# Kernel tuning notes

Measured on AMD Instinct MI355X. Metric: run time of the kernel, lower is better.

Reference implementation:

```python
import jax, jax.numpy as jnp
import numpy as np
import math

NUM_HEADS = 16
ROPE_BASE = 10000.0
SLIDING_WINDOW = 512  # note: original triu-then-tril composition makes the mask empty (no-op)


def _rope_cos_sin(seq_len, head_dim, dtype):
    inv_freq = 1.0 / (ROPE_BASE ** (jnp.arange(0, head_dim, 2, dtype=jnp.float32) / head_dim))
    t = jnp.arange(seq_len, dtype=jnp.float32)
    freqs = t[:, None] * inv_freq[None, :]          # [S, D/2]
    emb = jnp.concatenate([freqs, freqs], axis=-1)  # [S, D]
    # reshape to broadcast over [B, S, H, D]
    return jnp.cos(emb)[None, :, None, :].astype(dtype), jnp.sin(emb)[None, :, None, :].astype(dtype)


def _rotate_half(x):
    x1, x2 = jnp.split(x, 2, axis=-1)
    return jnp.concatenate([-x2, x1], axis=-1)


def setup_inputs() -> dict:
    key = jax.random.key(0)
    ks = jax.random.split(key, 9)
    B, S, E = 2, 2048, 2048
    sc = 1.0 / math.sqrt(E)
    return {
        "hidden_states": jax.random.normal(ks[0], (B, S, E), dtype=jnp.float32),
        "Wq": jax.random.normal(ks[1], (E, E), dtype=jnp.float32) * sc,
        "bq": jax.random.normal(ks[2], (E,), dtype=jnp.float32) * 0.01,
        "Wk": jax.random.normal(ks[3], (E, E), dtype=jnp.float32) * sc,
        "bk": jax.random.normal(ks[4], (E,), dtype=jnp.float32) * 0.01,
        "Wv": jax.random.normal(ks[5], (E, E), dtype=jnp.float32) * sc,
        "bv": jax.random.normal(ks[6], (E,), dtype=jnp.float32) * 0.01,
        "Wo": jax.random.normal(ks[7], (E, E), dtype=jnp.float32) * sc,
        "bo": jax.random.normal(ks[8], (E,), dtype=jnp.float32) * 0.01,
    }


def reference(hidden_states, Wq, bq, Wk, bk, Wv, bv, Wo, bo):
    B, S, E = hidden_states.shape
    H = NUM_HEADS
    D = E // H
    q = (hidden_states @ Wq.T + bq).reshape(B, S, H, D)
    k = (hidden_states @ Wk.T + bk).reshape(B, S, H, D)
    v = (hidden_states @ Wv.T + bv).reshape(B, S, H, D)

    cos, sin = _rope_cos_sin(S, D, q.dtype)
    q = q * cos + _rotate_half(q) * sin
    k = k * cos + _rotate_half(k) * sin

    scale = 1.0 / math.sqrt(D)
    scores = jnp.einsum("bqhd,bkhd->bhqk", q, k) * scale  # [B,H,S,S]
    # Faithful to source: triu(ones, +w) followed by tril(..., -w) is empty -> mask is a no-op.
    attn = jax.nn.softmax(scores, axis=-1)
    out = jnp.einsum("bhqk,bkhd->bqhd", attn, v).reshape(B, S, E)
    return out @ Wo.T + bo
```

## Files before the change

### kernel.cpp

```cpp
#include <hip/hip_runtime.h>
#include <hip/hip_bf16.h>

#define B_ 2
#define S_ 2048
#define E_ 2048
#define H_ 16
#define D_ 128
#define M_ (B_*S_)
#define NQKV_ (3*E_)

typedef __attribute__((ext_vector_type(8))) short bf16x8;
typedef __attribute__((ext_vector_type(4))) float f32x4;
typedef __attribute__((ext_vector_type(4))) unsigned short u16x4;
typedef __attribute__((ext_vector_type(2))) unsigned u32x2;

__device__ __forceinline__ unsigned short f2bf(float f) {
  union { float f; unsigned u; } v; v.f = f;
  unsigned r = v.u + 0x7fffu + ((v.u >> 16) & 1u);
  return (unsigned short)(r >> 16);
}
__device__ __forceinline__ float bf2f(unsigned short h) {
  union { unsigned u; float f; } v; v.u = ((unsigned)h) << 16;
  return v.f;
}

__device__ __forceinline__ void gload_lds16(const void* g, void* l) {
  __builtin_amdgcn_global_load_lds(
      (const __attribute__((address_space(1))) unsigned*)g,
      (__attribute__((address_space(3))) unsigned*)l, 16, 0, 0);
}

__global__ __launch_bounds__(256) void prep_kernel(
    const float* __restrict__ hs,
    const float* __restrict__ Wq, const float* __restrict__ Wk, const float* __restrict__ Wv,
    const float* __restrict__ Wo,
    const float* __restrict__ bq, const float* __restrict__ bk, const float* __restrict__ bv,
    unsigned short* __restrict__ hsb, unsigned short* __restrict__ Wqkv,
    unsigned short* __restrict__ Wob, float* __restrict__ biasqkv,
    float* __restrict__ cosT, float* __restrict__ sinT)
{
  const int seg = blockIdx.y;
  const int t0 = blockIdx.x * 256 + threadIdx.x;
  const int stride = gridDim.x * 256;
  if (seg == 0) {
    const int n = (M_*E_)/4;
    for (int i = t0; i < n; i += stride) {
      f32x4 v = ((const f32x4*)hs)[i];
      u16x4 o; o[0]=f2bf(v[0]); o[1]=f2bf(v[1]); o[2]=f2bf(v[2]); o[3]=f2bf(v[3]);
      ((u16x4*)hsb)[i] = o;
    }
  } else if (seg == 1) {
    const int n = (3*E_*E_)/4;
    for (int i = t0; i < n; i += stride) {
      int e4 = i << 2;
      int r = e4 >> 11;
      int k = e4 & 2047;
      const float* src = (r < E_) ? (Wq + ((size_t)r << 11) + k)
                       : (r < 2*E_) ? (Wk + ((size_t)(r - E_) << 11) + k)
                       : (Wv + ((size_t)(r - 2*E_) << 11) + k);
      f32x4 v = *(const f32x4*)src;
      u16x4 o; o[0]=f2bf(v[0]); o[1]=f2bf(v[1]); o[2]=f2bf(v[2]); o[3]=f2bf(v[3]);
      ((u16x4*)Wqkv)[i] = o;
    }
  } else if (seg == 2) {
    const int n = (E_*E_)/4;
    for (int i = t0; i < n; i += stride) {
      f32x4 v = ((const f32x4*)Wo)[i];
      u16x4 o; o[0]=f2bf(v[0]); o[1]=f2bf(v[1]); o[2]=f2bf(v[2]); o[3]=f2bf(v[3]);
      ((u16x4*)Wob)[i] = o;
    }
  } else if (seg == 3) {
    for (int i = t0; i < NQKV_; i += stride)
      biasqkv[i] = (i < E_) ? bq[i] : (i < 2*E_) ? bk[i - E_] : bv[i - 2*E_];
  } else {
    for (int i = t0; i < S_*64; i += stride) {
      int j = i & 63, s = i >> 6;
      float inv = exp2f(-(float)j * (13.287712379549449f / 64.0f));
      float ang = (float)s * inv;
      cosT[i] = cosf(ang);
      sinT[i] = sinf(ang);
    }
  }
}

#define STAGE8(basePtr, BUF, AB, KS, KT) do { \
    unsigned short* dst_ = lds + (BUF)*32768 + (AB)*16384 + (KS)*8192; \
    const unsigned short* src_ = (basePtr) + (KT)*64 + (KS)*32; \
    _Pragma("unroll") \
    for (int j_ = 0; j_ < 2; ++j_) { \
      int cc_ = (j_ << 9) + tid; \
      int row_ = cc_ >> 2, c2_ = cc_ & 3; \
      int sc_ = c2_ ^ ((row_ >> 1) & 3); \
      gload_lds16(src_ + (size_t)row_*K + sc_*8, (char*)dst_ + cc_*16); \
    } } while(0)

#define LOADA8(DST, MH, KS, BUF) do { \
    const unsigned short* Ab_ = lds + (BUF)*32768 + (KS)*8192; \
    _Pragma("unroll") \
    for (int j_ = 0; j_ < 4; ++j_) { \
      int row_ = wr*128 + ((MH)*4 + j_)*16 + l15; \
      DST[j_] = *(const bf16x8*)(Ab_ + row_*32 + ((l4 ^ ((row_>>1)&3)) << 3)); \
    } } while(0)

#define LOADB8(DST, KS, BUF) do { \
    const unsigned short* Bb_ = lds + (BUF)*32768 + 16384 + (KS)*8192; \
    _Pragma("unroll") \
    for (int j_ = 0; j_ < 4; ++j_) { \
      int row_ = wc*64 + j_*16 + l15; \
      DST[j_] = *(const bf16x8*)(Bb_ + row_*32 + ((l4 ^ ((row_>>1)&3)) << 3)); \
    } } while(0)

#define PRIO_MFMA(MH, AF, BF) do { \
    __builtin_amdgcn_s_setprio(1); \
    _Pragma("unroll") \
    for (int mm_ = 0; mm_ < 4; ++mm_) \
      _Pragma("unroll") \
      for (int nn_ = 0; nn_ < 4; ++nn_) \
        acc[(MH)*4+mm_][nn_] = __builtin_amdgcn_mfma_f32_16x16x32_bf16(AF[mm_], BF[nn_], acc[(MH)*4+mm_][nn_], 0,0,0); \
    __builtin_amdgcn_s_setprio(0); \
  } while(0)

#define BARPIN do { \
    __builtin_amdgcn_sched_barrier(0); \
    __builtin_amdgcn_s_barrier(); \
    __builtin_amdgcn_sched_barrier(0); \
  } while(0)

__global__ __launch_bounds__(512, 2) void gemm8(
    const unsigned short* __restrict__ A,
    const unsigned short* __restrict__ Bm,
    const float* __restrict__ bias,
    unsigned short* __restrict__ Cv,
    int M, int N, int K)
{
  __shared__ __align__(16) unsigned short lds[65536];
  const int tid = threadIdx.x;
  const int lane = tid & 63;
  const int w = tid >> 6;
  const int wr = w >> 2, wc = w & 3;
  const int l15 = lane & 15, l4 = lane >> 4;

  const int ntile = N >> 8;
  int wg = blockIdx.x;
  const int cpx = gridDim.x >> 3;
  wg = (wg & 7) * cpx + (wg >> 3);
  const int tm = wg / ntile, tn = wg % ntile;

  const unsigned short* Abase = A + ((size_t)tm*256)*K;
  const unsigned short* Bbase = Bm + ((size_t)tn*256)*K;

  f32x4 acc[8][4] = {};
  bf16x8 afA[4], afB[4], bfA[4], bfB[4];

  const int NITER = K >> 7;

  STAGE8(Bbase, 0, 1, 0, 0); STAGE8(Abase, 0, 0, 0, 0);
  STAGE8(Bbase, 0, 1, 1, 0); STAGE8(Abase, 0, 0, 1, 0);
  STAGE8(Bbase, 1, 1, 0, 1); STAGE8(Abase, 1, 0, 0, 1);
  STAGE8(Bbase, 1, 1, 1, 1);
  __builtin_amdgcn_sched_barrier(0);
  asm volatile("s_waitcnt vmcnt(6)" ::: "memory");
  __builtin_amdgcn_s_barrier();
  __builtin_amdgcn_sched_barrier(0);

  for (int i = 0; i < NITER; ++i) {
    const int t1k = 2*i + 1, t2k = 2*i + 2, t3k = 2*i + 3;
    const bool nl = (i < NITER - 1);
    STAGE8(Abase, 1, 0, 1, t1k);
    LOADA8(afA, 0, 0, 0); LOADB8(bfA, 0, 0);
    LOADA8(afB, 1, 0, 0);
    PRIO_MFMA(0, afA, bfA);
    BARPIN;
    if (nl) STAGE8(Bbase, 0, 1, 0, t2k);
    LOADA8(afA, 0, 1, 0); LOADB8(bfB, 1, 0);
    PRIO_MFMA(1, afB, bfA);
    BARPIN;
    if (nl) STAGE8(Abase, 0, 0, 0, t2k);
    LOADA8(afB, 1, 1, 0);
    PRIO_MFMA(0, afA, bfB);
    BARPIN;
    if (nl) STAGE8(Bbase, 0, 1, 1, t2k);
    PRIO_MFMA(1, afB, bfB);
    __builtin_amdgcn_sched_barrier(0);
    if (nl) asm volatile("s_waitcnt vmcnt(6)" ::: "memory");
    else    asm volatile("s_waitcnt vmcnt(0)" ::: "memory");
    __builtin_amdgcn_s_barrier();
    __builtin_amdgcn_sched_barrier(0);
    if (nl) STAGE8(Abase, 0, 0, 1, t2k);
    LOADA8(afA, 0, 0, 1); LOADB8(bfA, 0, 1);
    LOADA8(afB, 1, 0, 1);
    PRIO_MFMA(0, afA, bfA);
    BARPIN;
    if (nl) STAGE8(Bbase, 1, 1, 0, t3k);
    LOADA8(afA, 0, 1, 1); LOADB8(bfB, 1, 1);
    PRIO_MFMA(1, afB, bfA);
    BARPIN;
    if (nl) STAGE8(Abase, 1, 0, 0, t3k);
    LOADA8(afB, 1, 1, 1);
    PRIO_MFMA(0, afA, bfB);
    BARPIN;
    if (nl) STAGE8(Bbase, 1, 1, 1, t3k);
    PRIO_MFMA(1, afB, bfB);
    __builtin_amdgcn_sched_barrier(0);
    if (nl) asm volatile("s_waitcnt vmcnt(6)" ::: "memory");
    else    asm volatile("s_waitcnt vmcnt(0)" ::: "memory");
    __builtin_amdgcn_s_barrier();
    __builtin_amdgcn_sched_barrier(0);
  }

  #pragma unroll
  for (int mt = 0; mt < 8; ++mt) {
    #pragma unroll
    for (int nt = 0; nt < 4; ++nt) {
      int colg = tn*256 + wc*64 + nt*16 + l15;
      float bvv = bias[colg];
      #pragma unroll
      for (int r = 0; r < 4; ++r) {
        int rowg = tm*256 + wr*128 + mt*16 + l4*4 + r;
        Cv[(size_t)rowg*N + colg] = f2bf(acc[mt][nt][r] + bvv);
      }
    }
  }
}

template<int OUT_F32>
__global__ __launch_bounds__(256) void gemm_bt(
    const unsigned short* __restrict__ A,
    const unsigned short* __restrict__ Bm,
    const float* __restrict__ bias,
    void* __restrict__ Cv,
    int M, int N, int K)
{
  __shared__ unsigned short lA[128*64];
  __shared__ unsigned short lB[128*64];
  const int tid = threadIdx.x;
  const int lane = tid & 63;
  const int w = tid >> 6;
  const int wr = w >> 1, wc = w & 1;
  const int ntile = N >> 7;
  const int tm = blockIdx.x / ntile, tn = blockIdx.x % ntile;
  const int l15 = lane & 15, l4 = lane >> 4;

  f32x4 acc[4][4] = {};

  for (int kt = 0; kt < K; kt += 64) {
    #pragma unroll
    for (int i = 0; i < 4; ++i) {
      int cc = i*256 + tid;
      int row = cc >> 3, col = cc & 7;
      int scol = col ^ (row & 7);
      gload_lds16(A + (size_t)(tm*128 + row)*K + kt + scol*8, (char*)lA + cc*16);
    }
    #pragma unroll
    for (int i = 0; i < 4; ++i) {
      int cc = i*256 + tid;
      int row = cc >> 3, col = cc & 7;
      int scol = col ^ (row & 7);
      gload_lds16(Bm + (size_t)(tn*128 + row)*K + kt + scol*8, (char*)lB + cc*16);
    }
    asm volatile("s_waitcnt vmcnt(0)" ::: "memory");
    __syncthreads();

    #pragma unroll
    for (int ks = 0; ks < 2; ++ks) {
      bf16x8 af[4], bfr[4];
      #pragma unroll
      for (int mt = 0; mt < 4; ++mt) {
        int row = wr*64 + mt*16 + l15;
        int ch = (ks*4 + l4) ^ (row & 7);
        af[mt] = *(const bf16x8*)(lA + row*64 + ch*8);
      }
      #pragma unroll
      for (int nt = 0; nt < 4; ++nt) {
        int row = wc*64 + nt*16 + l15;
        int ch = (ks*4 + l4) ^ (row & 7);
        bfr[nt] = *(const bf16x8*)(lB + row*64 + ch*8);
      }
      #pragma unroll
      for (int mt = 0; mt < 4; ++mt)
        #pragma unroll
        for (int nt = 0; nt < 4; ++nt)
          acc[mt][nt] = __builtin_amdgcn_mfma_f32_16x16x32_bf16(af[mt], bfr[nt], acc[mt][nt], 0, 0, 0);
    }
    __syncthreads();
  }

  #pragma unroll
  for (int mt = 0; mt < 4; ++mt) {
    #pragma unroll
    for (int nt = 0; nt < 4; ++nt) {
      int colg = tn*128 + wc*64 + nt*16 + l15;
      float bvv = bias[colg];
      #pragma unroll
      for (int r = 0; r < 4; ++r) {
        int rowg = tm*128 + wr*64 + mt*16 + l4*4 + r;
        float v = acc[mt][nt][r] + bvv;
        if (OUT_F32) ((float*)Cv)[(size_t)rowg*N + colg] = v;
        else ((unsigned short*)Cv)[(size_t)rowg*N + colg] = f2bf(v);
      }
    }
  }
}

__global__ __launch_bounds__(256) void rope_kernel(
    unsigned short* __restrict__ qkv, const float* __restrict__ cosT, const float* __restrict__ sinT)
{
  int t = blockIdx.x*256 + threadIdx.x;
  int i  = t & 63;
  int h  = (t >> 6) & 15;
  int m  = t >> 10;
  int s  = m & (S_-1);
  float c = cosT[s*64 + i], sn = sinT[s*64 + i];
  const float scale = 0.08838834764831845f * 1.4426950408889634f;
  size_t base = (size_t)m*NQKV_ + h*128;
  float q1 = bf2f(qkv[base+i]), q2 = bf2f(qkv[base+64+i]);
  qkv[base+i]    = f2bf((q1*c - q2*sn)*scale);
  qkv[base+64+i] = f2bf((q2*c + q1*sn)*scale);
  size_t kb = base + E_;
  float k1 = bf2f(qkv[kb+i]), k2 = bf2f(qkv[kb+64+i]);
  qkv[kb+i]    = f2bf(k1*c - k2*sn);
  qkv[kb+64+i] = f2bf(k2*c + k1*sn);
}

__global__ __launch_bounds__(256) void transv_kernel(
    const unsigned short* __restrict__ qkv, unsigned short* __restrict__ Vt)
{
  __shared__ unsigned short t[32][33];
  int bid = blockIdx.x;
  int st = bid & 63;
  int dt = (bid >> 6) & 3;
  int bh = bid >> 8;
  int b = bh >> 4, h = bh & 15;
  int tx = threadIdx.x & 31, ty = threadIdx.x >> 5;
  #pragma unroll
  for (int j = 0; j < 4; ++j) {
    int r = ty + j*8;
    t[r][tx] = qkv[(size_t)(b*S_ + st*32 + r)*NQKV_ + 2*E_ + h*128 + dt*32 + tx];
  }
  __syncthreads();
  #pragma unroll
  for (int j = 0; j < 4; ++j) {
    int r = ty + j*8;
    Vt[((size_t)bh*D_ + dt*32 + r)*S_ + st*32 + tx] = t[tx][r];
  }
}

__global__ __launch_bounds__(256, 4) void attn_kernel(
    const unsigned short* __restrict__ qkv, const unsigned short* __restrict__ Vt,
    unsigned short* __restrict__ Ao)
{
  __shared__ unsigned short lK[64*128];
  __shared__ unsigned short lV[128*64];
  __shared__ __align__(16) unsigned short lP[4*16*64];
  const int bid = blockIdx.x;
  const int qt = bid & 31;
  const int bh = bid >> 5;
  const int b = bh >> 4, h = bh & 15;
  const int tid = threadIdx.x, lane = tid & 63, w = tid >> 6;
  const int l15 = lane & 15, l4 = lane >> 4;

  const int qrow = qt*64 + w*16 + l15;
  const unsigned short* qp = qkv + (size_t)(b*S_ + qrow)*NQKV_ + h*128 + l4*8;
  bf16x8 qf[4];
  #pragma unroll
  for (int f = 0; f < 4; ++f) qf[f] = *(const bf16x8*)(qp + f*32);

  f32x4 O[8];
  #pragma unroll
  for (int i = 0; i < 8; ++i) O[i] = (f32x4){0.f,0.f,0.f,0.f};
  float m = -1e30f, lsum = 0.f;

  unsigned short* myP = lP + w*(16*64);
  const int ksw = (l15 & 7) << 3;
  const size_t kbase = (size_t)b*S_*NQKV_ + E_ + (size_t)h*128;
  const size_t vbase = (size_t)bh*D_*S_;

  for (int kt = 0; kt < S_; kt += 64) {
    #pragma unroll
    for (int i = 0; i < 4; ++i) {
      int cc = i*256 + tid;
      int row = cc >> 4, col = cc & 15;
      int scol = col ^ (row & 7);
      gload_lds16(qkv + kbase + (size_t)(kt + row)*NQKV_ + scol*8, (char*)lK + cc*16);
    }
    #pragma unroll
    for (int i = 0; i < 4; ++i) {
      int cc = i*256 + tid;
      int row = cc >> 3, col = cc & 7;
      int scol = col ^ ((row & 7) ^ ((row >> 3) & 7));
      gload_lds16(Vt + vbase + (size_t)row*S_ + kt + scol*8, (char*)lV + cc*16);
    }
    asm volatile("s_waitcnt vmcnt(0)" ::: "memory");
    __syncthreads();

    f32x4 sfr[4];
    #pragma unroll
    for (int nf = 0; nf < 4; ++nf) {
      f32x4 s = (f32x4){0.f,0.f,0.f,0.f};
      #pragma unroll
      for (int ks = 0; ks < 4; ++ks) {
        int row = nf*16 + l15;
        int ch = (ks*4 + l4) ^ (row & 7);
        bf16x8 kf = *(const bf16x8*)(lK + row*128 + ch*8);
        s = __builtin_amdgcn_mfma_f32_16x16x32_bf16(kf, qf[ks], s, 0, 0, 0);
      }
      sfr[nf] = s;
    }

    float vmax = -1e30f;
    #pragma unroll
    for (int nf = 0; nf < 4; ++nf)
      #pragma unroll
      for (int r = 0; r < 4; ++r) vmax = fmaxf(vmax, sfr[nf][r]);
    vmax = fmaxf(vmax, __shfl_xor(vmax, 16, 64));
    vmax = fmaxf(vmax, __shfl_xor(vmax, 32, 64));

    if (__any(vmax > m + 8.0f)) {
      float mn = fmaxf(m, vmax);
      float al = __builtin_amdgcn_exp2f(m - mn);
      m = mn;
      lsum *= al;
      #pragma unroll
      for (int r = 0; r < 4; ++r) {
        float ar = __shfl(al, (lane & 48) + l4*4 + r, 64);
        #pragma unroll
        for (int df = 0; df < 8; ++df) O[df][r] *= ar;
      }
    }

    float ps = 0.f;
    #pragma unroll
    for (int nf = 0; nf < 4; ++nf) {
      #pragma unroll
      for (int r = 0; r < 4; ++r) {
        float p = __builtin_amdgcn_exp2f(sfr[nf][r] - m);
        sfr[nf][r] = p;
        ps += p;
      }
    }
    ps += __shfl_xor(ps, 16, 64);
    ps += __shfl_xor(ps, 32, 64);
    lsum += ps;

    #pragma unroll
    for (int nf = 0; nf < 4; ++nf) {
      unsigned lo = (unsigned)f2bf(sfr[nf][0]) | ((unsigned)f2bf(sfr[nf][1]) << 16);
      unsigned hi = (unsigned)f2bf(sfr[nf][2]) | ((unsigned)f2bf(sfr[nf][3]) << 16);
      int k0 = (nf*16 + l4*4) ^ ksw;
      u32x2 val; val[0] = lo; val[1] = hi;
      *(u32x2*)(myP + l15*64 + k0) = val;
    }
    asm volatile("s_waitcnt lgkmcnt(0)" ::: "memory");

    #pragma unroll
    for (int ks2 = 0; ks2 < 2; ++ks2) {
      int kk = (ks2*32 + l4*8) ^ ksw;
      bf16x8 pf = *(const bf16x8*)(myP + l15*64 + kk);
      #pragma unroll
      for (int df = 0; df < 8; ++df) {
        int row = df*16 + l15;
        int ch = (ks2*4 + l4) ^ ((row & 7) ^ ((row >> 3) & 7));
        bf16x8 vf = *(const bf16x8*)(lV + row*64 + ch*8);
        O[df] = __builtin_amdgcn_mfma_f32_16x16x32_bf16(pf, vf, O[df], 0, 0, 0);
      }
    }
    __syncthreads();
  }

  float linv = 1.0f / lsum;
  float inv[4];
  #pragma unroll
  for (int r = 0; r < 4; ++r) inv[r] = __shfl(linv, (lane & 48) + l4*4 + r, 64);
  #pragma unroll
  for (int df = 0; df < 8; ++df) {
    int colg = h*128 + df*16 + l15;
    #pragma unroll
    for (int r = 0; r < 4; ++r) {
      int rowg = qt*64 + w*16 + l4*4 + r;
      Ao[(size_t)(b*S_ + rowg)*E_ + colg] = f2bf(O[df][r] * inv[r]);
    }
  }
}

extern "C" void kernel_launch(void* const* d_in, const int* in_sizes, int n_in,
                              void* d_out, int out_size, void* d_ws, size_t ws_size,
                              hipStream_t stream) {
  const float* hs = (const float*)d_in[0];
  const float* Wq = (const float*)d_in[1];
  const float* bq = (const float*)d_in[2];
  const float* Wk = (const float*)d_in[3];
  const float* bk = (const float*)d_in[4];
  const float* Wv = (const float*)d_in[5];
  const float* bv = (const float*)d_in[6];
  const float* Wo = (const float*)d_in[7];
  const float* bo = (const float*)d_in[8];
  float* out = (float*)d_out;

  char* p = (char*)d_ws;
  auto alloc = [&](size_t bytes) { char* r = p; p += (bytes + 255) & ~(size_t)255; return r; };
  unsigned short* hsb  = (unsigned short*)alloc((size_t)M_*E_*2);
  unsigned short* Wqkv = (unsigned short*)alloc((size_t)NQKV_*E_*2);
  unsigned short* Wob  = (unsigned short*)alloc((size_t)E_*E_*2);
  unsigned short* qkv  = (unsigned short*)alloc((size_t)M_*NQKV_*2);
  unsigned short* Vt   = (unsigned short*)alloc((size_t)B_*H_*D_*S_*2);
  unsigned short* Ao   = (unsigned short*)alloc((size_t)M_*E_*2);
  float* biasqkv = (float*)alloc((size_t)NQKV_*4);
  float* cosT = (float*)alloc((size_t)S_*64*4);
  float* sinT = (float*)alloc((size_t)S_*64*4);

  prep_kernel<<<dim3(2048, 5), 256, 0, stream>>>(hs, Wq, Wk, Wv, Wo, bq, bk, bv,
      hsb, Wqkv, Wob, biasqkv, cosT, sinT);
  gemm8<<<dim3((M_/256)*(NQKV_/256)), 512, 0, stream>>>(hsb, Wqkv, biasqkv, qkv, M_, NQKV_, E_);
  rope_kernel<<<dim3((M_*H_*64)/256), 256, 0, stream>>>(qkv, cosT, sinT);
  transv_kernel<<<dim3(B_*H_*(D_/32)*(S_/32)), 256, 0, stream>>>(qkv, Vt);
  attn_kernel<<<dim3(B_*H_*(S_/64)), 256, 0, stream>>>(qkv, Vt, Ao);
  gemm_bt<1><<<dim3((M_/128)*(E_/128)), 256, 0, stream>>>(Ao, Wob, bo, out, M_, E_, E_);
}
```

Before: 318.1 us.

## Double attention query tile per block to reuse K/V LDS tiles

Each wave now processes two 16-row query groups instead of one, so a block covers 128 query rows and every K/V tile loaded into LDS feeds twice the MFMA work. This halves the global-to-LDS traffic per query row and the number of blocks. The block index is also remapped so that consecutive blocks are spread across heads. In exchange, register use roughly doubles, launch bounds drop from 4 to 2 waves per SIMD, and only 512 blocks are launched, which lowers occupancy and latency hiding.

```diff
diff --git a/kernel.cpp b/kernel.cpp
--- a/kernel.cpp
+++ b/kernel.cpp
@@ -345,32 +345,38 @@
   }
 }
 
-__global__ __launch_bounds__(256, 4) void attn_kernel(
+__global__ __launch_bounds__(256, 2) void attn_kernel(
     const unsigned short* __restrict__ qkv, const unsigned short* __restrict__ Vt,
     unsigned short* __restrict__ Ao)
 {
   __shared__ unsigned short lK[64*128];
   __shared__ unsigned short lV[128*64];
-  __shared__ __align__(16) unsigned short lP[4*16*64];
-  const int bid = blockIdx.x;
-  const int qt = bid & 31;
-  const int bh = bid >> 5;
+  __shared__ __align__(16) unsigned short lP[4*32*64];
+  int bid = blockIdx.x;
+  bid = (bid & 7)*64 + (bid >> 3);
+  const int qt = bid & 15;
+  const int bh = bid >> 4;
   const int b = bh >> 4, h = bh & 15;
   const int tid = threadIdx.x, lane = tid & 63, w = tid >> 6;
   const int l15 = lane & 15, l4 = lane >> 4;
 
-  const int qrow = qt*64 + w*16 + l15;
-  const unsigned short* qp = qkv + (size_t)(b*S_ + qrow)*NQKV_ + h*128 + l4*8;
-  bf16x8 qf[4];
-  #pragma unroll
-  for (int f = 0; f < 4; ++f) qf[f] = *(const bf16x8*)(qp + f*32);
-
-  f32x4 O[8];
-  #pragma unroll
-  for (int i = 0; i < 8; ++i) O[i] = (f32x4){0.f,0.f,0.f,0.f};
-  float m = -1e30f, lsum = 0.f;
-
-  unsigned short* myP = lP + w*(16*64);
+  bf16x8 qf[2][4];
+  #pragma unroll
+  for (int g = 0; g < 2; ++g) {
+    const int qrow = qt*128 + w*32 + g*16 + l15;
+    const unsigned short* qp = qkv + (size_t)(b*S_ + qrow)*NQKV_ + h*128 + l4*8;
+    #pragma unroll
+    for (int f = 0; f < 4; ++f) qf[g][f] = *(const bf16x8*)(qp + f*32);
+  }
+
+  f32x4 O[2][8];
+  #pragma unroll
+  for (int g = 0; g < 2; ++g)
+    #pragma unroll
+    for (int i = 0; i < 8; ++i) O[g][i] = (f32x4){0.f,0.f,0.f,0.f};
+  float mx[2] = {-1e30f,-1e30f}, lsum[2] = {0.f,0.f};
+
+  unsigned short* myP = lP + w*(32*64);
   const int ksw = (l15 & 7) << 3;
   const size_t kbase = (size_t)b*S_*NQKV_ + E_ + (size_t)h*128;
   const size_t vbase = (size_t)bh*D_*S_;
@@ -393,91 +399,112 @@
     asm volatile("s_waitcnt vmcnt(0)" ::: "memory");
     __syncthreads();
 
-    f32x4 sfr[4];
+    f32x4 sfr[2][4];
     #pragma unroll
     for (int nf = 0; nf < 4; ++nf) {
-      f32x4 s = (f32x4){0.f,0.f,0.f,0.f};
+      f32x4 s0 = (f32x4){0.f,0.f,0.f,0.f};
+      f32x4 s1 = (f32x4){0.f,0.f,0.f,0.f};
       #pragma unroll
       for (int ks = 0; ks < 4; ++ks) {
         int row = nf*16 + l15;
         int ch = (ks*4 + l4) ^ (row & 7);
         bf16x8 kf = *(const bf16x8*)(lK + row*128 + ch*8);
-        s = __builtin_amdgcn_mfma_f32_16x16x32_bf16(kf, qf[ks], s, 0, 0, 0);
-      }
-      sfr[nf] = s;
-    }
-
-    float vmax = -1e30f;
-    #pragma unroll
-    for (int nf = 0; nf < 4; ++nf)
-      #pragma unroll
-      for (int r = 0; r < 4; ++r) vmax = fmaxf(vmax, sfr[nf][r]);
-    vmax = fmaxf(vmax, __shfl_xor(vmax, 16, 64));
-    vmax = fmaxf(vmax, __shfl_xor(vmax, 32, 64));
-
-    if (__any(vmax > m + 8.0f)) {
-      float mn = fmaxf(m, vmax);
-      float al = __builtin_amdgcn_exp2f(m - mn);
-      m = mn;
-      lsum *= al;
-      #pragma unroll
-      for (int r = 0; r < 4; ++r) {
-        float ar = __shfl(al, (lane & 48) + l4*4 + r, 64);
+        s0 = __builtin_amdgcn_mfma_f32_16x16x32_bf16(kf, qf[0][ks], s0, 0, 0, 0);
+        s1 = __builtin_amdgcn_mfma_f32_16x16x32_bf16(kf, qf[1][ks], s1, 0, 0, 0);
+      }
+      sfr[0][nf] = s0; sfr[1][nf] = s1;
+    }
+
+    float vm[2];
+    #pragma unroll
+    for (int g = 0; g < 2; ++g) {
+      float v = -1e30f;
+      #pragma unroll
+      for (int nf = 0; nf < 4; ++nf)
         #pragma unroll
-        for (int df = 0; df < 8; ++df) O[df][r] *= ar;
-      }
-    }
-
-    float ps = 0.f;
-    #pragma unroll
-    for (int nf = 0; nf < 4; ++nf) {
-      #pragma unroll
-      for (int r = 0; r < 4; ++r) {
-        float p = __builtin_amdgcn_exp2f(sfr[nf][r] - m);
-        sfr[nf][r] = p;
-        ps += p;
-      }
-    }
-    ps += __shfl_xor(ps, 16, 64);
-    ps += __shfl_xor(ps, 32, 64);
-    lsum += ps;
-
-    #pragma unroll
-    for (int nf = 0; nf < 4; ++nf) {
-      unsigned lo = (unsigned)f2bf(sfr[nf][0]) | ((unsigned)f2bf(sfr[nf][1]) << 16);
-      unsigned hi = (unsigned)f2bf(sfr[nf][2]) | ((unsigned)f2bf(sfr[nf][3]) << 16);
-      int k0 = (nf*16 + l4*4) ^ ksw;
-      u32x2 val; val[0] = lo; val[1] = hi;
-      *(u32x2*)(myP + l15*64 + k0) = val;
+        for (int r = 0; r < 4; ++r) v = fmaxf(v, sfr[g][nf][r]);
+      v = fmaxf(v, __shfl_xor(v, 16, 64));
+      v = fmaxf(v, __shfl_xor(v, 32, 64));
+      vm[g] = v;
+    }
+
+    if (__any((vm[0] > mx[0] + 8.0f) || (vm[1] > mx[1] + 8.0f))) {
+      #pragma unroll
+      for (int g = 0; g < 2; ++g) {
+        float mn = fmaxf(mx[g], vm[g]);
+        float al = __builtin_amdgcn_exp2f(mx[g] - mn);
+        mx[g] = mn;
+        lsum[g] *= al;
+        #pragma unroll
+        for (int r = 0; r < 4; ++r) {
+          float ar = __shfl(al, (lane & 48) + l4*4 + r, 64);
+          #pragma unroll
+          for (int df = 0; df < 8; ++df) O[g][df][r] *= ar;
+        }
+      }
+    }
+
+    #pragma unroll
+    for (int g = 0; g < 2; ++g) {
+      float ps = 0.f;
+      #pragma unroll
+      for (int nf = 0; nf < 4; ++nf) {
+        #pragma unroll
+        for (int r = 0; r < 4; ++r) {
+          float p = __builtin_amdgcn_exp2f(sfr[g][nf][r] - mx[g]);
+          sfr[g][nf][r] = p;
+          ps += p;
+        }
+      }
+      ps += __shfl_xor(ps, 16, 64);
+      ps += __shfl_xor(ps, 32, 64);
+      lsum[g] += ps;
+    }
+
+    #pragma unroll
+    for (int g = 0; g < 2; ++g) {
+      #pragma unroll
+      for (int nf = 0; nf < 4; ++nf) {
+        unsigned lo = (unsigned)f2bf(sfr[g][nf][0]) | ((unsigned)f2bf(sfr[g][nf][1]) << 16);
+        unsigned hi = (unsigned)f2bf(sfr[g][nf][2]) | ((unsigned)f2bf(sfr[g][nf][3]) << 16);
+        int k0 = (nf*16 + l4*4) ^ ksw;
+        u32x2 val; val[0] = lo; val[1] = hi;
+        *(u32x2*)(myP + (g*16 + l15)*64 + k0) = val;
+      }
     }
     asm volatile("s_waitcnt lgkmcnt(0)" ::: "memory");
 
     #pragma unroll
     for (int ks2 = 0; ks2 < 2; ++ks2) {
       int kk = (ks2*32 + l4*8) ^ ksw;
-      bf16x8 pf = *(const bf16x8*)(myP + l15*64 + kk);
+      bf16x8 pf0 = *(const bf16x8*)(myP + l15*64 + kk);
+      bf16x8 pf1 = *(const bf16x8*)(myP + (16 + l15)*64 + kk);
       #pragma unroll
       for (int df = 0; df < 8; ++df) {
         int row = df*16 + l15;
         int ch = (ks2*4 + l4) ^ ((row & 7) ^ ((row >> 3) & 7));
         bf16x8 vf = *(const bf16x8*)(lV + row*64 + ch*8);
-        O[df] = __builtin_amdgcn_mfma_f32_16x16x32_bf16(pf, vf, O[df], 0, 0, 0);
+        O[0][df] = __builtin_amdgcn_mfma_f32_16x16x32_bf16(pf0, vf, O[0][df], 0, 0, 0);
+        O[1][df] = __builtin_amdgcn_mfma_f32_16x16x32_bf16(pf1, vf, O[1][df], 0, 0, 0);
       }
     }
     __syncthreads();
   }
 
-  float linv = 1.0f / lsum;
-  float inv[4];
-  #pragma unroll
-  for (int r = 0; r < 4; ++r) inv[r] = __shfl(linv, (lane & 48) + l4*4 + r, 64);
-  #pragma unroll
-  for (int df = 0; df < 8; ++df) {
-    int colg = h*128 + df*16 + l15;
-    #pragma unroll
-    for (int r = 0; r < 4; ++r) {
-      int rowg = qt*64 + w*16 + l4*4 + r;
-      Ao[(size_t)(b*S_ + rowg)*E_ + colg] = f2bf(O[df][r] * inv[r]);
+  #pragma unroll
+  for (int g = 0; g < 2; ++g) {
+    float linv = 1.0f / lsum[g];
+    float inv[4];
+    #pragma unroll
+    for (int r = 0; r < 4; ++r) inv[r] = __shfl(linv, (lane & 48) + l4*4 + r, 64);
+    #pragma unroll
+    for (int df = 0; df < 8; ++df) {
+      int colg = h*128 + df*16 + l15;
+      #pragma unroll
+      for (int r = 0; r < 4; ++r) {
+        int rowg = qt*128 + w*32 + g*16 + l4*4 + r;
+        Ao[(size_t)(b*S_ + rowg)*E_ + colg] = f2bf(O[g][df][r] * inv[r]);
+      }
     }
   }
 }
@@ -513,6 +540,6 @@
   gemm8<<<dim3((M_/256)*(NQKV_/256)), 512, 0, stream>>>(hsb, Wqkv, biasqkv, qkv, M_, NQKV_, E_);
   rope_kernel<<<dim3((M_*H_*64)/256), 256, 0, stream>>>(qkv, cosT, sinT);
   transv_kernel<<<dim3(B_*H_*(D_/32)*(S_/32)), 256, 0, stream>>>(qkv, Vt);
-  attn_kernel<<<dim3(B_*H_*(S_/64)), 256, 0, stream>>>(qkv, Vt, Ao);
+  attn_kernel<<<dim3(B_*H_*(S_/128)), 256, 0, stream>>>(qkv, Vt, Ao);
   gemm_bt<1><<<dim3((M_/128)*(E_/128)), 256, 0, stream>>>(Ao, Wob, bo, out, M_, E_, E_);
 }
```

After: 296.0 us. 1.07x faster.
